# Performance work log

Measured on AMD Instinct MI355X. Metric: run time of the kernel, lower is better.

The kernel has to match this reference:

```python
import jax, jax.numpy as jnp
import numpy as np
from jax import lax

B, T, F = 64, 100, 128
HD = [32, 64]            # encoder hidden dims; decoder uses reversed [64, 32]
KH, KW = 3, 3


def _conv(x, w):
    # x: (b, cin, f, 1), w: (cout, cin, kh, kw), SAME padding
    ph, pw = w.shape[2] // 2, w.shape[3] // 2
    return lax.conv_general_dilated(x, w, (1, 1), [(ph, ph), (pw, pw)],
                                    dimension_numbers=("NCHW", "OIHW", "NCHW"))


def _run_layer(xs, h0, wg, bg, wc, bc):
    # xs: (t, b, cin, f, 1); h0: (b, hd, f, 1)
    def step(h, x):
        g = _conv(jnp.concatenate([x, h], axis=1), wg) + bg[None, :, None, None]
        r, u = jnp.split(jax.nn.sigmoid(g), 2, axis=1)
        c = jnp.tanh(_conv(jnp.concatenate([x, r * h], axis=1), wc) + bc[None, :, None, None])
        h_next = (1.0 - u) * h + u * c
        return h_next, h_next
    h_last, ys = lax.scan(step, h0, xs)
    return ys, h_last


def setup_inputs() -> dict:
    key = jax.random.key(0)
    ks = iter(jax.random.split(key, 32))
    s = 0.05
    d = {"x": jax.random.normal(next(ks), (B, T, F), dtype=jnp.float32)}
    # encoder: layer0 in=1 hd=32, layer1 in=32 hd=64
    # decoder: input_dim=64, hidden reversed [64,32]: layer0 in=64 hd=64, layer1 in=64 hd=32
    specs = {
        "e0": (1, 32), "e1": (32, 64),
        "d0": (64, 64), "d1": (64, 32),
    }
    for name, (cin, hd) in specs.items():
        d[name + "_wg"] = jax.random.normal(next(ks), (2 * hd, cin + hd, KH, KW), dtype=jnp.float32) * s
        d[name + "_bg"] = jnp.zeros((2 * hd,), dtype=jnp.float32)
        d[name + "_wc"] = jax.random.normal(next(ks), (hd, cin + hd, KH, KW), dtype=jnp.float32) * s
        d[name + "_bc"] = jnp.zeros((hd,), dtype=jnp.float32)
    d["fw"] = jax.random.normal(next(ks), (1, 32, 1, 1), dtype=jnp.float32) * s
    d["fb"] = jnp.zeros((1,), dtype=jnp.float32)
    return d


def reference(x,
              e0_wg, e0_bg, e0_wc, e0_bc,
              e1_wg, e1_bg, e1_wc, e1_bc,
              d0_wg, d0_bg, d0_wc, d0_bc,
              d1_wg, d1_bg, d1_wc, d1_bc,
              fw, fb):
    b, t, f = x.shape
    xs = x.reshape(b, t, 1, f, 1).transpose(1, 0, 2, 3, 4)  # (t,b,1,f,1)
    zeros = lambda hd: jnp.zeros((b, hd, f, 1), dtype=x.dtype)
    # encoder (return_all_layers; decoder consumes last layer output)
    y0, h0 = _run_layer(xs, zeros(HD[0]), e0_wg, e0_bg, e0_wc, e0_bc)
    y1, h1 = _run_layer(y0, zeros(HD[1]), e1_wg, e1_bg, e1_wc, e1_bc)
    # decoder init states = encoder last states reversed: [h1 (64ch), h0 (32ch)]
    z0, _ = _run_layer(y1, h1, d0_wg, d0_bg, d0_wc, d0_bc)
    z1, _ = _run_layer(z0, h0, d1_wg, d1_bg, d1_wc, d1_bc)
    # final 1x1 conv: (t,b,32,f,1) x (1,32) -> (t,b,1,f,1)
    rec = jnp.einsum("tbcfw,oc->tbofw", z1, fw[:, :, 0, 0]) + fb[None, None, :, None, None]
    return rec.transpose(1, 0, 2, 3, 4).reshape(b, t, f)
```

## Files before the change

kernel.cpp:

```cpp
#include <hip/hip_runtime.h>
#include <cstdint>
#include <cstddef>


#define F_ 128
#define T_ 100
#define B_ 64
#define ROWSP 130
#define CBSTR (ROWSP * 8)
#define CBBYTE (ROWSP * 16)
#define AT_OFF 104448
#define LDS_TOTAL (AT_OFF + 28 * CBBYTE)

typedef _Float16 f16;
typedef __attribute__((ext_vector_type(4))) float f32x4;
typedef __attribute__((ext_vector_type(8))) _Float16 f16x8;
typedef __attribute__((ext_vector_type(4))) _Float16 f16x4;

#define MFMA(a, b, c) __builtin_amdgcn_mfma_f32_16x16x32_f16(a, b, c, 0, 0, 0)

__device__ __forceinline__ float exp2_(float x) { return __builtin_amdgcn_exp2f(x); }
__device__ __forceinline__ float rcp_(float x) { return __builtin_amdgcn_rcpf(x); }

#define KSG (-1.442695041f)
#define KTH (-2.885390082f)

__host__ __device__ constexpr int cbA(int lid, int km) {
  return lid == 0 ? (km ? 4 : 0)
       : lid == 1 ? (1 + km * 4)
       : lid == 2 ? (km * 4)
                  : (8 + km * 4);
}
__host__ __device__ constexpr int cbB(int lid, int km) {
  return lid == 0 ? (km ? 17 : 13)
       : lid == 1 ? (km == 0 ? 1 : 14 + km * 4)
       : lid == 2 ? (km < 2 ? km * 4 : 12 + km * 4)
                  : (km < 2 ? 8 + km * 4 : 20);
}

template <int LID, int FTW, int NK, int NC3, bool WREG>
__device__ __forceinline__ void convA_f(
    const f16* __restrict__ rdB,
    const f16x8* __restrict__ aR, const f16x8* __restrict__ aU,
    const f16* __restrict__ gR, const f16* __restrict__ gU,
    f32x4* __restrict__ accR, f32x4* __restrict__ accU) {
#pragma unroll
  for (int j = 0; j < FTW; ++j) {
    accR[j] = (f32x4){0.f, 0.f, 0.f, 0.f};
    accU[j] = (f32x4){0.f, 0.f, 0.f, 0.f};
  }
#pragma unroll
  for (int ks = 0; ks < NK; ++ks) {
    const int k = ks / NC3, km = ks % NC3;
    const f16* fb = rdB + cbA(LID, km) * CBSTR + k * 8;
    f16x8 bf[FTW];
#pragma unroll
    for (int j = 0; j < FTW; ++j) bf[j] = *(const f16x8*)(fb + j * 128);
    f16x8 wr, wu;
    if constexpr (WREG) { wr = aR[ks]; wu = aU[ks]; }
    else {
      wr = *(const f16x8*)(gR + ks * 512);
      wu = *(const f16x8*)(gU + ks * 512);
    }
#pragma unroll
    for (int j = 0; j < FTW; ++j) accR[j] = MFMA(wr, bf[j], accR[j]);
#pragma unroll
    for (int j = 0; j < FTW; ++j) accU[j] = MFMA(wu, bf[j], accU[j]);
  }
}

template <int LID, int FTW, int NK, int NC3, bool CREG>
__device__ __forceinline__ void convB_f(
    const f16* __restrict__ rdB, const f16x8* __restrict__ cR,
    const f16* __restrict__ cW, f32x4* __restrict__ accC) {
#pragma unroll
  for (int j = 0; j < FTW; ++j) accC[j] = (f32x4){0.f, 0.f, 0.f, 0.f};
#pragma unroll
  for (int ks = 0; ks < NK; ++ks) {
    const int k = ks / NC3, km = ks % NC3;
    const f16* fb = rdB + cbB(LID, km) * CBSTR + k * 8;
    f16x8 bf[FTW];
#pragma unroll
    for (int j = 0; j < FTW; ++j) bf[j] = *(const f16x8*)(fb + j * 128);
    f16x8 wc;
    if constexpr (CREG) wc = cR[ks];
    else wc = *(const f16x8*)(cW + ks * 512);
#pragma unroll
    for (int j = 0; j < FTW; ++j) accC[j] = MFMA(wc, bf[j], accC[j]);
  }
}

template <int FTW, int RHCB>
__device__ __forceinline__ void postA_f(const f32x4* __restrict__ accR,
                                        const f32x4 bR,
                                        const f32x4* __restrict__ hreg,
                                        char* __restrict__ wrB) {
#pragma unroll
  for (int j = 0; j < FTW; ++j) {
    f16x4 rh;
#pragma unroll
    for (int q = 0; q < 4; ++q) {
      const float r = rcp_(1.0f + exp2_(fmaf(accR[j][q], KSG, bR[q])));
      rh[q] = (f16)(r * hreg[j][q]);
    }
    *(f16x4*)(wrB + RHCB * CBBYTE + j * 256) = rh;
  }
}

template <int FTW, int HCB, bool EMITY1>
__device__ __forceinline__ void postB_f(const f32x4* __restrict__ accU,
                                        const f32x4* __restrict__ accC,
                                        const f32x4 bU, const f32x4 bC,
                                        f32x4* __restrict__ hreg,
                                        char* __restrict__ wrB,
                                        f16* __restrict__ y1dst) {
#pragma unroll
  for (int j = 0; j < FTW; ++j) {
    f16x4 hh;
#pragma unroll
    for (int q = 0; q < 4; ++q) {
      const float u = rcp_(1.0f + exp2_(fmaf(accU[j][q], KSG, bU[q])));
      const float r = rcp_(1.0f + exp2_(fmaf(accC[j][q], KTH, bC[q])));
      const float h = hreg[j][q];
      const float s = fmaf(2.0f, r, -(1.0f + h));
      const float hn = fmaf(u, s, h);
      hreg[j][q] = hn;
      hh[q] = (f16)hn;
    }
    *(f16x4*)(wrB + HCB * CBBYTE + j * 256) = hh;
    if constexpr (EMITY1) *(f16x4*)(y1dst + j * 128) = hh;
  }
}

__global__ __launch_bounds__(512, 1) void ae_kernel(
    const f16* __restrict__ xf, float* __restrict__ out,
    const f16* __restrict__ wgE0, const f16* __restrict__ wcE0,
    const float* __restrict__ bgE0, const float* __restrict__ bcE0,
    const f16* __restrict__ wgE1, const f16* __restrict__ wcE1,
    const float* __restrict__ bgE1, const float* __restrict__ bcE1,
    const f16* __restrict__ wgD0, const f16* __restrict__ wcD0,
    const float* __restrict__ bgD0, const float* __restrict__ bcD0,
    const f16* __restrict__ wgD1, const f16* __restrict__ wcD1,
    const float* __restrict__ bgD1, const float* __restrict__ bcD1,
    const float* __restrict__ fw, const float* __restrict__ fb,
    f16* __restrict__ y1g) {
  extern __shared__ char smem[];
  f16* aT = (f16*)(smem + AT_OFF);
  const int tid = threadIdx.x, b = blockIdx.x;
  const int w = tid >> 6, l = tid & 63;
  const int m16 = l & 15, kb = l >> 4;

  for (int i = tid; i < 28 * CBBYTE / 16; i += 512)
    ((f32x4*)(smem + AT_OFF))[i] = (f32x4){0.f, 0.f, 0.f, 0.f};
  for (int i = tid; i < 1536; i += 512)
    ((f16x8*)(smem + 0))[i] = ((const f16x8*)wgE0)[i];
  for (int i = tid; i < 768; i += 512)
    ((f16x8*)(smem + 24576))[i] = ((const f16x8*)wcE0)[i];

  const int cot2 = w & 1, cot4 = w & 3;
  f16x8 aR1[9], aU1[9], cE1[9];
#pragma unroll
  for (int ks = 0; ks < 9; ++ks) {
    aR1[ks] = ((const f16x8*)wgE1)[(cot4 * 9 + ks) * 64 + l];
    aU1[ks] = ((const f16x8*)wgE1)[((cot4 + 4) * 9 + ks) * 64 + l];
    cE1[ks] = ((const f16x8*)wcE1)[(cot4 * 9 + ks) * 64 + l];
  }
  const int co2 = cot2 * 16 + kb * 4;
  const int co4 = cot4 * 16 + kb * 4;
  f32x4 bRe0, bUe0, bCe0, bRe1, bUe1, bCe1;
#pragma unroll
  for (int q = 0; q < 4; ++q) {
    bRe0[q] = bgE0[co2 + q] * KSG;
    bUe0[q] = bgE0[32 + co2 + q] * KSG;
    bCe0[q] = bcE0[co2 + q] * KTH;
    bRe1[q] = bgE1[co4 + q] * KSG;
    bUe1[q] = bgE1[64 + co4 + q] * KSG;
    bCe1[q] = bcE1[co4 + q] * KTH;
  }
  const int ft2 = (w >> 1) * 2, ft4 = (w >> 2) * 4;
  const f16* rdB2 = aT + kb * CBSTR + (ft2 * 16 + m16) * 8;
  const f16* rdB4 = aT + kb * CBSTR + (ft4 * 16 + m16) * 8;
  char* wrB2 = (char*)aT + (cot2 * 2 + (kb >> 1)) * CBBYTE +
               (ft2 * 16 + m16 + 1) * 16 + (kb & 1) * 8;
  char* wrB4 = (char*)aT + (cot4 * 2 + (kb >> 1)) * CBBYTE +
               (ft4 * 16 + m16 + 1) * 16 + (kb & 1) * 8;
  f16* y1t = y1g + (size_t)b * T_ * 8192 +
             ((cot4 * 2 + (kb >> 1)) * 128 + ft4 * 16 + m16) * 8 + (kb & 1) * 4;
  const f16* gE0R = (const f16*)(smem + 0) + (cot2 * 6) * 512 + l * 8;
  const f16* gE0U = (const f16*)(smem + 0) + ((2 + cot2) * 6) * 512 + l * 8;
  const f16* cE0l = (const f16*)(smem + 24576) + (cot2 * 6) * 512 + l * 8;

  f32x4 h0r[2], h1r[4];
#pragma unroll
  for (int j = 0; j < 2; ++j) h0r[j] = (f32x4){0.f, 0.f, 0.f, 0.f};
#pragma unroll
  for (int j = 0; j < 4; ++j) h1r[j] = (f32x4){0.f, 0.f, 0.f, 0.f};
  __syncthreads();

  const f16* xb = xf + (size_t)b * T_ * F_;
  if (tid < F_) {
    const f16 v = xb[tid];
    aT[(tid + 1) * 8] = v;
    aT[13 * CBSTR + (tid + 1) * 8] = v;
  }
  __syncthreads();
  for (int t = 0; t < T_; ++t) {
    f32x4 aR0g[2], aU0g[2];
    convA_f<0, 2, 6, 2, false>(rdB2, nullptr, nullptr, gE0R, gE0U, aR0g, aU0g);
    f16 xpre = (f16)0.f;
    if (t + 1 < T_ && tid < F_) xpre = xb[(t + 1) * F_ + tid];
    postA_f<2, 14>(aR0g, bRe0, h0r, wrB2);
    __syncthreads();
    f32x4 aC0[2];
    convB_f<0, 2, 6, 2, false>(rdB2, nullptr, cE0l, aC0);
    postB_f<2, 1, false>(aU0g, aC0, bUe0, bCe0, h0r, wrB2, nullptr);
    __syncthreads();
    f32x4 aR1g[4], aU1g[4];
    convA_f<1, 4, 9, 3, true>(rdB4, aR1, aU1, nullptr, nullptr, aR1g, aU1g);
    if (t + 1 < T_ && tid < F_) {
      aT[(tid + 1) * 8] = xpre;
      aT[13 * CBSTR + (tid + 1) * 8] = xpre;
    }
    postA_f<4, 18>(aR1g, bRe1, h1r, wrB4);
    __syncthreads();
    f32x4 aC1[4];
    convB_f<1, 4, 9, 3, true>(rdB4, cE1, nullptr, aC1);
    postB_f<4, 5, true>(aU1g, aC1, bUe1, bCe1, h1r, wrB4,
                        y1t + (size_t)t * 8192);
    __syncthreads();
  }

  {
#pragma unroll
    for (int j = 0; j < 4; ++j) {
      f16x4 hh;
#pragma unroll
      for (int q = 0; q < 4; ++q) hh[q] = (f16)h1r[j][q];
      *(f16x4*)(wrB4 + 8 * CBBYTE + j * 256) = hh;
    }
#pragma unroll
    for (int j = 0; j < 2; ++j) {
      f16x4 hh;
#pragma unroll
      for (int q = 0; q < 4; ++q) hh[q] = (f16)h0r[j][q];
      *(f16x4*)(wrB2 + 16 * CBBYTE + j * 256) = hh;
    }
  }
  for (int i = tid; i < 3072; i += 512)
    ((f16x8*)(smem + 0))[i] = ((const f16x8*)wcD0)[i];
  for (int i = tid; i < 2304; i += 512)
    ((f16x8*)(smem + 49152))[i] = ((const f16x8*)wgD1)[i];
  for (int i = tid; i < 1152; i += 512)
    ((f16x8*)(smem + 86016))[i] = ((const f16x8*)wcD1)[i];
  f16x8 aR0[12], aU0[12];
#pragma unroll
  for (int ks = 0; ks < 12; ++ks) {
    aR0[ks] = ((const f16x8*)wgD0)[(cot4 * 12 + ks) * 64 + l];
    aU0[ks] = ((const f16x8*)wgD0)[((cot4 + 4) * 12 + ks) * 64 + l];
  }
  f32x4 bRd0, bUd0, bCd0, bRd1, bUd1, bCd1;
#pragma unroll
  for (int q = 0; q < 4; ++q) {
    bRd0[q] = bgD0[co4 + q] * KSG;
    bUd0[q] = bgD0[64 + co4 + q] * KSG;
    bCd0[q] = bcD0[co4 + q] * KTH;
    bRd1[q] = bgD1[co2 + q] * KSG;
    bUd1[q] = bgD1[32 + co2 + q] * KSG;
    bCd1[q] = bcD1[co2 + q] * KTH;
  }
  const f16* cD0l = (const f16*)(smem + 0) + (cot4 * 12) * 512 + l * 8;
  const f16* gD1R = (const f16*)(smem + 49152) + (cot2 * 9) * 512 + l * 8;
  const f16* gD1U = (const f16*)(smem + 49152) + ((2 + cot2) * 9) * 512 + l * 8;
  const f16* cD1l = (const f16*)(smem + 86016) + (cot2 * 9) * 512 + l * 8;
  const float fb0 = fb[0];
  __syncthreads();
  {
    const f16x8* src = (const f16x8*)(y1g + (size_t)b * T_ * 8192);
#pragma unroll
    for (int k2 = 0; k2 < 2; ++k2) {
      const int i = tid + k2 * 512;
      *(f16x8*)&aT[(i >> 7) * CBSTR + ((i & 127) + 1) * 8] = src[i];
    }
  }
  __syncthreads();

  for (int t = 0; t < T_; ++t) {
    f32x4 aRd0[4], aUd0[4];
    convA_f<2, 4, 12, 4, true>(rdB4, aR0, aU0, nullptr, nullptr, aRd0, aUd0);
    if (t >= 1 && tid < F_) {
      float s = fb0;
#pragma unroll
      for (int cb = 0; cb < 4; ++cb) {
        const f16x8 h8 = *(const f16x8*)&aT[(16 + cb) * CBSTR + (tid + 1) * 8];
#pragma unroll
        for (int q = 0; q < 8; ++q) s = fmaf(fw[cb * 8 + q], (float)h8[q], s);
      }
      out[((size_t)b * T_ + (t - 1)) * F_ + tid] = s;
    }
    f16x8 yp0 = {}, yp1 = {};
    if (t + 1 < T_) {
      const f16x8* src = (const f16x8*)(y1g + ((size_t)b * T_ + t + 1) * 8192);
      yp0 = src[tid];
      yp1 = src[tid + 512];
    }
    postA_f<4, 20>(aRd0, bRd0, h1r, wrB4);
    __syncthreads();
    f32x4 aCd0[4];
    convB_f<2, 4, 12, 4, false>(rdB4, nullptr, cD0l, aCd0);
    postB_f<4, 8, false>(aUd0, aCd0, bUd0, bCd0, h1r, wrB4, nullptr);
    __syncthreads();
    f32x4 aRd1[2], aUd1[2];
    convA_f<3, 2, 9, 3, false>(rdB2, nullptr, nullptr, gD1R, gD1U, aRd1, aUd1);
    if (t + 1 < T_) {
      const int i0 = tid, i1 = tid + 512;
      *(f16x8*)&aT[(i0 >> 7) * CBSTR + ((i0 & 127) + 1) * 8] = yp0;
      *(f16x8*)&aT[(i1 >> 7) * CBSTR + ((i1 & 127) + 1) * 8] = yp1;
    }
    postA_f<2, 20>(aRd1, bRd1, h0r, wrB2);
    __syncthreads();
    f32x4 aCd1[2];
    convB_f<3, 2, 9, 3, false>(rdB2, nullptr, cD1l, aCd1);
    postB_f<2, 16, false>(aUd1, aCd1, bUd1, bCd1, h0r, wrB2, nullptr);
    __syncthreads();
  }
  if (tid < F_) {
    float s = fb0;
#pragma unroll
    for (int cb = 0; cb < 4; ++cb) {
      const f16x8 h8 = *(const f16x8*)&aT[(16 + cb) * CBSTR + (tid + 1) * 8];
#pragma unroll
      for (int q = 0; q < 8; ++q) s = fmaf(fw[cb * 8 + q], (float)h8[q], s);
    }
    out[((size_t)b * T_ + (T_ - 1)) * F_ + tid] = s;
  }
}

__global__ void repack_f16(const float* __restrict__ src, f16* __restrict__ dst,
                           int CO, int CI, int CINH, int NK, int e0map) {
  const int n = (CO / 16) * NK * 64;
  for (int i = blockIdx.x * blockDim.x + threadIdx.x; i < n;
       i += gridDim.x * blockDim.x) {
    const int cot = i / (NK * 64);
    const int r = i - cot * NK * 64;
    const int ks = r >> 6, lph = r & 63;
    const int co = cot * 16 + (lph & 15);
    const int kbl = lph >> 4;
#pragma unroll
    for (int j = 0; j < 8; ++j) {
      const int kk = ks * 32 + kbl * 8 + j;
      const int k = kk / CINH, c = kk - k * CINH;
      int ci;
      if (e0map) ci = (c == 0) ? 0 : ((c >= 8 && c < 40) ? c - 7 : -1);
      else ci = (c < CI) ? c : -1;
      float wv = 0.f;
      if (ci >= 0) wv = src[((size_t)(co * CI + ci) * 3 + k) * 3 + 1];
      dst[(size_t)i * 8 + j] = (f16)wv;
    }
  }
}

__global__ void xcvt(const float* __restrict__ x, f16* __restrict__ xf, int n4) {
  for (int i = blockIdx.x * blockDim.x + threadIdx.x; i < n4;
       i += gridDim.x * blockDim.x) {
    const float4 v = ((const float4*)x)[i];
    f16x4 o;
    o[0] = (f16)v.x; o[1] = (f16)v.y; o[2] = (f16)v.z; o[3] = (f16)v.w;
    ((f16x4*)xf)[i] = o;
  }
}

extern "C" void kernel_launch(void* const* d_in, const int* in_sizes, int n_in,
                              void* d_out, int out_size, void* d_ws, size_t ws_size,
                              hipStream_t stream) {
  (void)in_sizes; (void)n_in; (void)out_size; (void)ws_size;
  const float* x = (const float*)d_in[0];
  const float* e0_wg = (const float*)d_in[1];
  const float* e0_bg = (const float*)d_in[2];
  const float* e0_wc = (const float*)d_in[3];
  const float* e0_bc = (const float*)d_in[4];
  const float* e1_wg = (const float*)d_in[5];
  const float* e1_bg = (const float*)d_in[6];
  const float* e1_wc = (const float*)d_in[7];
  const float* e1_bc = (const float*)d_in[8];
  const float* d0_wg = (const float*)d_in[9];
  const float* d0_bg = (const float*)d_in[10];
  const float* d0_wc = (const float*)d_in[11];
  const float* d0_bc = (const float*)d_in[12];
  const float* d1_wg = (const float*)d_in[13];
  const float* d1_bg = (const float*)d_in[14];
  const float* d1_wc = (const float*)d_in[15];
  const float* d1_bc = (const float*)d_in[16];
  const float* fw = (const float*)d_in[17];
  const float* fb = (const float*)d_in[18];
  float* out = (float*)d_out;

  char* p = (char*)d_ws;
  f16* y1g = (f16*)p;
  p += (size_t)B_ * T_ * 64 * 128 * 2;
  f16* xf = (f16*)p;
  p += (size_t)B_ * T_ * F_ * 2;
  auto aw = [&](int n) { f16* q = (f16*)p; p += (size_t)n * 2; return q; };
  f16* wgE0 = aw(64 * 192);
  f16* wcE0 = aw(32 * 192);
  f16* wgE1 = aw(128 * 288);
  f16* wcE1 = aw(64 * 288);
  f16* wgD0 = aw(128 * 384);
  f16* wcD0 = aw(64 * 384);
  f16* wgD1 = aw(64 * 288);
  f16* wcD1 = aw(32 * 288);

  auto rp = [&](const float* s, f16* d, int CO, int CI, int CINH, int e0m) {
    const int NK = 3 * CINH / 32;
    const int n = (CO / 16) * NK * 64;
    hipLaunchKernelGGL(repack_f16, dim3((n + 255) / 256), dim3(256), 0, stream,
                       s, d, CO, CI, CINH, NK, e0m);
  };
  rp(e0_wg, wgE0, 64, 33, 64, 1);
  rp(e0_wc, wcE0, 32, 33, 64, 1);
  rp(e1_wg, wgE1, 128, 96, 96, 0);
  rp(e1_wc, wcE1, 64, 96, 96, 0);
  rp(d0_wg, wgD0, 128, 128, 128, 0);
  rp(d0_wc, wcD0, 64, 128, 128, 0);
  rp(d1_wg, wgD1, 64, 96, 96, 0);
  rp(d1_wc, wcD1, 32, 96, 96, 0);
  hipLaunchKernelGGL(xcvt, dim3(200), dim3(1024), 0, stream, x, xf,
                     B_ * T_ * F_ / 4);

  hipFuncSetAttribute((const void*)ae_kernel,
                      hipFuncAttributeMaxDynamicSharedMemorySize, LDS_TOTAL);
  hipLaunchKernelGGL(ae_kernel, dim3(B_), dim3(512), LDS_TOTAL, stream, xf, out,
                     wgE0, wcE0, e0_bg, e0_bc, wgE1, wcE1, e1_bg, e1_bc,
                     wgD0, wcD0, d0_bg, d0_bc, wgD1, wcD1, d1_bg, d1_bc,
                     fw, fb, y1g);
}
```

Measured before the change: 1.166 ms.

## Skew layer pipelines to merge candidate phase of one layer with next step's gate phase

Within each of the encoder and decoder loops, the candidate conv and update of the second layer are deferred into the next timestep so they run in the same barrier phase as the first layer's gate conv. This cuts barriers per timestep from four to three. The r*h buffers are relocated to extra LDS channel blocks so both phases can coexist. The decoder layer-1 candidate weights move from LDS into registers, which raises register pressure. The skew needs a prologue/epilogue step and careful buffer separation to stay correct.

Result: slower. 1.280 ms (+9.7%).

```diff
diff --git a/kernel.cpp b/kernel.cpp
--- a/kernel.cpp
+++ b/kernel.cpp
@@ -9,8 +9,9 @@
 #define ROWSP 130
 #define CBSTR (ROWSP * 8)
 #define CBBYTE (ROWSP * 16)
-#define AT_OFF 104448
-#define LDS_TOTAL (AT_OFF + 28 * CBBYTE)
+#define AT_OFF 86016
+#define NCB 32
+#define LDS_TOTAL (AT_OFF + NCB * CBBYTE)
 
 typedef _Float16 f16;
 typedef __attribute__((ext_vector_type(4))) float f32x4;
@@ -27,15 +28,15 @@
 
 __host__ __device__ constexpr int cbA(int lid, int km) {
   return lid == 0 ? (km ? 4 : 0)
-       : lid == 1 ? (1 + km * 4)
-       : lid == 2 ? (km * 4)
-                  : (8 + km * 4);
+       : lid == 1 ? (km == 0 ? 1 : 4 + 4 * km)
+       : lid == 2 ? (4 * km)
+                  : (8 + 4 * km);
 }
 __host__ __device__ constexpr int cbB(int lid, int km) {
-  return lid == 0 ? (km ? 17 : 13)
-       : lid == 1 ? (km == 0 ? 1 : 14 + km * 4)
-       : lid == 2 ? (km < 2 ? km * 4 : 12 + km * 4)
-                  : (km < 2 ? 8 + km * 4 : 20);
+  return lid == 0 ? (km ? 20 : 16)
+       : lid == 1 ? (km == 0 ? 1 : 20 + 4 * km)
+       : lid == 2 ? (km < 2 ? 4 * km : 12 + 4 * km)
+                  : (km < 2 ? 8 + 4 * km : 28);
 }
 
 template <int LID, int FTW, int NK, int NC3, bool WREG>
@@ -150,7 +151,7 @@
   const int w = tid >> 6, l = tid & 63;
   const int m16 = l & 15, kb = l >> 4;
 
-  for (int i = tid; i < 28 * CBBYTE / 16; i += 512)
+  for (int i = tid; i < NCB * CBBYTE / 16; i += 512)
     ((f32x4*)(smem + AT_OFF))[i] = (f32x4){0.f, 0.f, 0.f, 0.f};
   for (int i = tid; i < 1536; i += 512)
     ((f16x8*)(smem + 0))[i] = ((const f16x8*)wgE0)[i];
@@ -201,43 +202,38 @@
   if (tid < F_) {
     const f16 v = xb[tid];
     aT[(tid + 1) * 8] = v;
-    aT[13 * CBSTR + (tid + 1) * 8] = v;
-  }
-  __syncthreads();
+    aT[16 * CBSTR + (tid + 1) * 8] = v;
+  }
+  __syncthreads();
+  f32x4 aU1g[4], aR1g[4];
   for (int t = 0; t < T_; ++t) {
-    f32x4 aR0g[2], aU0g[2];
+    f32x4 aC1[4], aR0g[2], aU0g[2];
+    if (t > 0) convB_f<1, 4, 9, 3, true>(rdB4, cE1, nullptr, aC1);
     convA_f<0, 2, 6, 2, false>(rdB2, nullptr, nullptr, gE0R, gE0U, aR0g, aU0g);
+    if (t > 0)
+      postB_f<4, 8, true>(aU1g, aC1, bUe1, bCe1, h1r, wrB4,
+                          y1t + (size_t)(t - 1) * 8192);
+    postA_f<2, 17>(aR0g, bRe0, h0r, wrB2);
+    __syncthreads();
+    f32x4 aC0[2];
+    convB_f<0, 2, 6, 2, false>(rdB2, nullptr, cE0l, aC0);
     f16 xpre = (f16)0.f;
     if (t + 1 < T_ && tid < F_) xpre = xb[(t + 1) * F_ + tid];
-    postA_f<2, 14>(aR0g, bRe0, h0r, wrB2);
-    __syncthreads();
-    f32x4 aC0[2];
-    convB_f<0, 2, 6, 2, false>(rdB2, nullptr, cE0l, aC0);
     postB_f<2, 1, false>(aU0g, aC0, bUe0, bCe0, h0r, wrB2, nullptr);
     __syncthreads();
-    f32x4 aR1g[4], aU1g[4];
     convA_f<1, 4, 9, 3, true>(rdB4, aR1, aU1, nullptr, nullptr, aR1g, aU1g);
     if (t + 1 < T_ && tid < F_) {
       aT[(tid + 1) * 8] = xpre;
-      aT[13 * CBSTR + (tid + 1) * 8] = xpre;
-    }
-    postA_f<4, 18>(aR1g, bRe1, h1r, wrB4);
-    __syncthreads();
+      aT[16 * CBSTR + (tid + 1) * 8] = xpre;
+    }
+    postA_f<4, 24>(aR1g, bRe1, h1r, wrB4);
+    __syncthreads();
+  }
+  {
     f32x4 aC1[4];
     convB_f<1, 4, 9, 3, true>(rdB4, cE1, nullptr, aC1);
-    postB_f<4, 5, true>(aU1g, aC1, bUe1, bCe1, h1r, wrB4,
-                        y1t + (size_t)t * 8192);
-    __syncthreads();
-  }
-
-  {
-#pragma unroll
-    for (int j = 0; j < 4; ++j) {
-      f16x4 hh;
-#pragma unroll
-      for (int q = 0; q < 4; ++q) hh[q] = (f16)h1r[j][q];
-      *(f16x4*)(wrB4 + 8 * CBBYTE + j * 256) = hh;
-    }
+    postB_f<4, 8, true>(aU1g, aC1, bUe1, bCe1, h1r, wrB4,
+                        y1t + (size_t)(T_ - 1) * 8192);
 #pragma unroll
     for (int j = 0; j < 2; ++j) {
       f16x4 hh;
@@ -246,18 +242,21 @@
       *(f16x4*)(wrB2 + 16 * CBBYTE + j * 256) = hh;
     }
   }
+  __syncthreads();
+
   for (int i = tid; i < 3072; i += 512)
     ((f16x8*)(smem + 0))[i] = ((const f16x8*)wcD0)[i];
   for (int i = tid; i < 2304; i += 512)
     ((f16x8*)(smem + 49152))[i] = ((const f16x8*)wgD1)[i];
-  for (int i = tid; i < 1152; i += 512)
-    ((f16x8*)(smem + 86016))[i] = ((const f16x8*)wcD1)[i];
-  f16x8 aR0[12], aU0[12];
+  f16x8 aR0[12], aU0[12], wCd1[9];
 #pragma unroll
   for (int ks = 0; ks < 12; ++ks) {
     aR0[ks] = ((const f16x8*)wgD0)[(cot4 * 12 + ks) * 64 + l];
     aU0[ks] = ((const f16x8*)wgD0)[((cot4 + 4) * 12 + ks) * 64 + l];
   }
+#pragma unroll
+  for (int ks = 0; ks < 9; ++ks)
+    wCd1[ks] = ((const f16x8*)wcD1)[(cot2 * 9 + ks) * 64 + l];
   f32x4 bRd0, bUd0, bCd0, bRd1, bUd1, bCd1;
 #pragma unroll
   for (int q = 0; q < 4; ++q) {
@@ -268,10 +267,9 @@
     bUd1[q] = bgD1[32 + co2 + q] * KSG;
     bCd1[q] = bcD1[co2 + q] * KTH;
   }
-  const f16* cD0l = (const f16*)(smem + 0) + (cot4 * 12) * 512 + l * 8;
   const f16* gD1R = (const f16*)(smem + 49152) + (cot2 * 9) * 512 + l * 8;
   const f16* gD1U = (const f16*)(smem + 49152) + ((2 + cot2) * 9) * 512 + l * 8;
-  const f16* cD1l = (const f16*)(smem + 86016) + (cot2 * 9) * 512 + l * 8;
+  const f16* cD0l = (const f16*)(smem + 0) + (cot4 * 12) * 512 + l * 8;
   const float fb0 = fb[0];
   __syncthreads();
   {
@@ -284,45 +282,49 @@
   }
   __syncthreads();
 
+  f32x4 aUd1[2], aRd1[2];
   for (int t = 0; t < T_; ++t) {
-    f32x4 aRd0[4], aUd0[4];
+    f32x4 aCd1[2], aRd0[4], aUd0[4];
+    if (t > 0) convB_f<3, 2, 9, 3, true>(rdB2, wCd1, nullptr, aCd1);
     convA_f<2, 4, 12, 4, true>(rdB4, aR0, aU0, nullptr, nullptr, aRd0, aUd0);
-    if (t >= 1 && tid < F_) {
-      float s = fb0;
-#pragma unroll
-      for (int cb = 0; cb < 4; ++cb) {
-        const f16x8 h8 = *(const f16x8*)&aT[(16 + cb) * CBSTR + (tid + 1) * 8];
-#pragma unroll
-        for (int q = 0; q < 8; ++q) s = fmaf(fw[cb * 8 + q], (float)h8[q], s);
-      }
-      out[((size_t)b * T_ + (t - 1)) * F_ + tid] = s;
-    }
     f16x8 yp0 = {}, yp1 = {};
     if (t + 1 < T_) {
       const f16x8* src = (const f16x8*)(y1g + ((size_t)b * T_ + t + 1) * 8192);
       yp0 = src[tid];
       yp1 = src[tid + 512];
     }
+    if (t > 0) postB_f<2, 16, false>(aUd1, aCd1, bUd1, bCd1, h0r, wrB2, nullptr);
     postA_f<4, 20>(aRd0, bRd0, h1r, wrB4);
     __syncthreads();
     f32x4 aCd0[4];
     convB_f<2, 4, 12, 4, false>(rdB4, nullptr, cD0l, aCd0);
+    if (t >= 1 && tid < F_) {
+      float s = fb0;
+#pragma unroll
+      for (int cb = 0; cb < 4; ++cb) {
+        const f16x8 h8 = *(const f16x8*)&aT[(16 + cb) * CBSTR + (tid + 1) * 8];
+#pragma unroll
+        for (int q = 0; q < 8; ++q) s = fmaf(fw[cb * 8 + q], (float)h8[q], s);
+      }
+      out[((size_t)b * T_ + (t - 1)) * F_ + tid] = s;
+    }
     postB_f<4, 8, false>(aUd0, aCd0, bUd0, bCd0, h1r, wrB4, nullptr);
     __syncthreads();
-    f32x4 aRd1[2], aUd1[2];
     convA_f<3, 2, 9, 3, false>(rdB2, nullptr, nullptr, gD1R, gD1U, aRd1, aUd1);
     if (t + 1 < T_) {
       const int i0 = tid, i1 = tid + 512;
       *(f16x8*)&aT[(i0 >> 7) * CBSTR + ((i0 & 127) + 1) * 8] = yp0;
       *(f16x8*)&aT[(i1 >> 7) * CBSTR + ((i1 & 127) + 1) * 8] = yp1;
     }
-    postA_f<2, 20>(aRd1, bRd1, h0r, wrB2);
-    __syncthreads();
+    postA_f<2, 28>(aRd1, bRd1, h0r, wrB2);
+    __syncthreads();
+  }
+  {
     f32x4 aCd1[2];
-    convB_f<3, 2, 9, 3, false>(rdB2, nullptr, cD1l, aCd1);
+    convB_f<3, 2, 9, 3, true>(rdB2, wCd1, nullptr, aCd1);
     postB_f<2, 16, false>(aUd1, aCd1, bUd1, bCd1, h0r, wrB2, nullptr);
-    __syncthreads();
-  }
+  }
+  __syncthreads();
   if (tid < F_) {
     float s = fb0;
 #pragma unroll
```

## Double block to 1024 threads and halve frequency tiles per wave

Applied to the files above, without the earlier changes.

The block size goes from 512 to 1024 threads, and each wave now handles half as many frequency tiles in every GRU layer step. The per-layer register arrays, tile offsets and staging loops are rescaled to match. This is meant to shorten the serial per-timestep critical path, since only 64 blocks run and each block's recurrence is latency-bound. In exchange, more waves share each CU's register file while the large register-resident weight fragments stay the same size, so register spilling or lower ILP is a risk, and barriers now synchronize twice as many waves.

After: 2.092 ms. +79.4%, slower.

```diff
diff --git a/kernel.cpp b/kernel.cpp
--- a/kernel.cpp
+++ b/kernel.cpp
@@ -132,7 +132,7 @@
   }
 }
 
-__global__ __launch_bounds__(512, 1) void ae_kernel(
+__global__ __launch_bounds__(1024, 1) void ae_kernel(
     const f16* __restrict__ xf, float* __restrict__ out,
     const f16* __restrict__ wgE0, const f16* __restrict__ wcE0,
     const float* __restrict__ bgE0, const float* __restrict__ bcE0,
@@ -150,14 +150,16 @@
   const int w = tid >> 6, l = tid & 63;
   const int m16 = l & 15, kb = l >> 4;
 
-  for (int i = tid; i < 28 * CBBYTE / 16; i += 512)
+  for (int i = tid; i < 28 * CBBYTE / 16; i += 1024)
     ((f32x4*)(smem + AT_OFF))[i] = (f32x4){0.f, 0.f, 0.f, 0.f};
-  for (int i = tid; i < 1536; i += 512)
+  for (int i = tid; i < 1536; i += 1024)
     ((f16x8*)(smem + 0))[i] = ((const f16x8*)wgE0)[i];
-  for (int i = tid; i < 768; i += 512)
+  for (int i = tid; i < 768; i += 1024)
     ((f16x8*)(smem + 24576))[i] = ((const f16x8*)wcE0)[i];
 
   const int cot2 = w & 1, cot4 = w & 3;
+  const int ft1 = w >> 1;
+  const int ftg2 = w >> 2;
   f16x8 aR1[9], aU1[9], cE1[9];
 #pragma unroll
   for (int ks = 0; ks < 9; ++ks) {
@@ -177,24 +179,22 @@
     bUe1[q] = bgE1[64 + co4 + q] * KSG;
     bCe1[q] = bcE1[co4 + q] * KTH;
   }
-  const int ft2 = (w >> 1) * 2, ft4 = (w >> 2) * 4;
-  const f16* rdB2 = aT + kb * CBSTR + (ft2 * 16 + m16) * 8;
-  const f16* rdB4 = aT + kb * CBSTR + (ft4 * 16 + m16) * 8;
+  const f16* rdB2 = aT + kb * CBSTR + (ft1 * 16 + m16) * 8;
+  const f16* rdB4 = aT + kb * CBSTR + (ftg2 * 32 + m16) * 8;
   char* wrB2 = (char*)aT + (cot2 * 2 + (kb >> 1)) * CBBYTE +
-               (ft2 * 16 + m16 + 1) * 16 + (kb & 1) * 8;
+               (ft1 * 16 + m16 + 1) * 16 + (kb & 1) * 8;
   char* wrB4 = (char*)aT + (cot4 * 2 + (kb >> 1)) * CBBYTE +
-               (ft4 * 16 + m16 + 1) * 16 + (kb & 1) * 8;
+               (ftg2 * 32 + m16 + 1) * 16 + (kb & 1) * 8;
   f16* y1t = y1g + (size_t)b * T_ * 8192 +
-             ((cot4 * 2 + (kb >> 1)) * 128 + ft4 * 16 + m16) * 8 + (kb & 1) * 4;
+             ((cot4 * 2 + (kb >> 1)) * 128 + ftg2 * 32 + m16) * 8 + (kb & 1) * 4;
   const f16* gE0R = (const f16*)(smem + 0) + (cot2 * 6) * 512 + l * 8;
   const f16* gE0U = (const f16*)(smem + 0) + ((2 + cot2) * 6) * 512 + l * 8;
   const f16* cE0l = (const f16*)(smem + 24576) + (cot2 * 6) * 512 + l * 8;
 
-  f32x4 h0r[2], h1r[4];
-#pragma unroll
-  for (int j = 0; j < 2; ++j) h0r[j] = (f32x4){0.f, 0.f, 0.f, 0.f};
-#pragma unroll
-  for (int j = 0; j < 4; ++j) h1r[j] = (f32x4){0.f, 0.f, 0.f, 0.f};
+  f32x4 h0r[1], h1r[2];
+  h0r[0] = (f32x4){0.f, 0.f, 0.f, 0.f};
+#pragma unroll
+  for (int j = 0; j < 2; ++j) h1r[j] = (f32x4){0.f, 0.f, 0.f, 0.f};
   __syncthreads();
 
   const f16* xb = xf + (size_t)b * T_ * F_;
@@ -205,52 +205,51 @@
   }
   __syncthreads();
   for (int t = 0; t < T_; ++t) {
-    f32x4 aR0g[2], aU0g[2];
-    convA_f<0, 2, 6, 2, false>(rdB2, nullptr, nullptr, gE0R, gE0U, aR0g, aU0g);
+    f32x4 aR0g[1], aU0g[1];
+    convA_f<0, 1, 6, 2, false>(rdB2, nullptr, nullptr, gE0R, gE0U, aR0g, aU0g);
     f16 xpre = (f16)0.f;
     if (t + 1 < T_ && tid < F_) xpre = xb[(t + 1) * F_ + tid];
-    postA_f<2, 14>(aR0g, bRe0, h0r, wrB2);
-    __syncthreads();
-    f32x4 aC0[2];
-    convB_f<0, 2, 6, 2, false>(rdB2, nullptr, cE0l, aC0);
-    postB_f<2, 1, false>(aU0g, aC0, bUe0, bCe0, h0r, wrB2, nullptr);
-    __syncthreads();
-    f32x4 aR1g[4], aU1g[4];
-    convA_f<1, 4, 9, 3, true>(rdB4, aR1, aU1, nullptr, nullptr, aR1g, aU1g);
+    postA_f<1, 14>(aR0g, bRe0, h0r, wrB2);
+    __syncthreads();
+    f32x4 aC0[1];
+    convB_f<0, 1, 6, 2, false>(rdB2, nullptr, cE0l, aC0);
+    postB_f<1, 1, false>(aU0g, aC0, bUe0, bCe0, h0r, wrB2, nullptr);
+    __syncthreads();
+    f32x4 aR1g[2], aU1g[2];
+    convA_f<1, 2, 9, 3, true>(rdB4, aR1, aU1, nullptr, nullptr, aR1g, aU1g);
     if (t + 1 < T_ && tid < F_) {
       aT[(tid + 1) * 8] = xpre;
       aT[13 * CBSTR + (tid + 1) * 8] = xpre;
     }
-    postA_f<4, 18>(aR1g, bRe1, h1r, wrB4);
-    __syncthreads();
-    f32x4 aC1[4];
-    convB_f<1, 4, 9, 3, true>(rdB4, cE1, nullptr, aC1);
-    postB_f<4, 5, true>(aU1g, aC1, bUe1, bCe1, h1r, wrB4,
+    postA_f<2, 18>(aR1g, bRe1, h1r, wrB4);
+    __syncthreads();
+    f32x4 aC1[2];
+    convB_f<1, 2, 9, 3, true>(rdB4, cE1, nullptr, aC1);
+    postB_f<2, 5, true>(aU1g, aC1, bUe1, bCe1, h1r, wrB4,
                         y1t + (size_t)t * 8192);
     __syncthreads();
   }
 
   {
 #pragma unroll
-    for (int j = 0; j < 4; ++j) {
+    for (int j = 0; j < 2; ++j) {
       f16x4 hh;
 #pragma unroll
       for (int q = 0; q < 4; ++q) hh[q] = (f16)h1r[j][q];
       *(f16x4*)(wrB4 + 8 * CBBYTE + j * 256) = hh;
     }
-#pragma unroll
-    for (int j = 0; j < 2; ++j) {
+    {
       f16x4 hh;
 #pragma unroll
-      for (int q = 0; q < 4; ++q) hh[q] = (f16)h0r[j][q];
-      *(f16x4*)(wrB2 + 16 * CBBYTE + j * 256) = hh;
-    }
-  }
-  for (int i = tid; i < 3072; i += 512)
+      for (int q = 0; q < 4; ++q) hh[q] = (f16)h0r[0][q];
+      *(f16x4*)(wrB2 + 16 * CBBYTE) = hh;
+    }
+  }
+  for (int i = tid; i < 3072; i += 1024)
     ((f16x8*)(smem + 0))[i] = ((const f16x8*)wcD0)[i];
-  for (int i = tid; i < 2304; i += 512)
+  for (int i = tid; i < 2304; i += 1024)
     ((f16x8*)(smem + 49152))[i] = ((const f16x8*)wgD1)[i];
-  for (int i = tid; i < 1152; i += 512)
+  for (int i = tid; i < 1152; i += 1024)
     ((f16x8*)(smem + 86016))[i] = ((const f16x8*)wcD1)[i];
   f16x8 aR0[12], aU0[12];
 #pragma unroll
@@ -276,17 +275,13 @@
   __syncthreads();
   {
     const f16x8* src = (const f16x8*)(y1g + (size_t)b * T_ * 8192);
-#pragma unroll
-    for (int k2 = 0; k2 < 2; ++k2) {
-      const int i = tid + k2 * 512;
-      *(f16x8*)&aT[(i >> 7) * CBSTR + ((i & 127) + 1) * 8] = src[i];
-    }
+    *(f16x8*)&aT[(tid >> 7) * CBSTR + ((tid & 127) + 1) * 8] = src[tid];
   }
   __syncthreads();
 
   for (int t = 0; t < T_; ++t) {
-    f32x4 aRd0[4], aUd0[4];
-    convA_f<2, 4, 12, 4, true>(rdB4, aR0, aU0, nullptr, nullptr, aRd0, aUd0);
+    f32x4 aRd0[2], aUd0[2];
+    convA_f<2, 2, 12, 4, true>(rdB4, aR0, aU0, nullptr, nullptr, aRd0, aUd0);
     if (t >= 1 && tid < F_) {
       float s = fb0;
 #pragma unroll
@@ -297,30 +292,26 @@
       }
       out[((size_t)b * T_ + (t - 1)) * F_ + tid] = s;
     }
-    f16x8 yp0 = {}, yp1 = {};
+    f16x8 yp0 = {};
     if (t + 1 < T_) {
       const f16x8* src = (const f16x8*)(y1g + ((size_t)b * T_ + t + 1) * 8192);
       yp0 = src[tid];
-      yp1 = src[tid + 512];
-    }
-    postA_f<4, 20>(aRd0, bRd0, h1r, wrB4);
-    __syncthreads();
-    f32x4 aCd0[4];
-    convB_f<2, 4, 12, 4, false>(rdB4, nullptr, cD0l, aCd0);
-    postB_f<4, 8, false>(aUd0, aCd0, bUd0, bCd0, h1r, wrB4, nullptr);
-    __syncthreads();
-    f32x4 aRd1[2], aUd1[2];
-    convA_f<3, 2, 9, 3, false>(rdB2, nullptr, nullptr, gD1R, gD1U, aRd1, aUd1);
-    if (t + 1 < T_) {
-      const int i0 = tid, i1 = tid + 512;
-      *(f16x8*)&aT[(i0 >> 7) * CBSTR + ((i0 & 127) + 1) * 8] = yp0;
-      *(f16x8*)&aT[(i1 >> 7) * CBSTR + ((i1 & 127) + 1) * 8] = yp1;
-    }
-    postA_f<2, 20>(aRd1, bRd1, h0r, wrB2);
-    __syncthreads();
-    f32x4 aCd1[2];
-    convB_f<3, 2, 9, 3, false>(rdB2, nullptr, cD1l, aCd1);
-    postB_f<2, 16, false>(aUd1, aCd1, bUd1, bCd1, h0r, wrB2, nullptr);
+    }
+    postA_f<2, 20>(aRd0, bRd0, h1r, wrB4);
+    __syncthreads();
+    f32x4 aCd0[2];
+    convB_f<2, 2, 12, 4, false>(rdB4, nullptr, cD0l, aCd0);
+    postB_f<2, 8, false>(aUd0, aCd0, bUd0, bCd0, h1r, wrB4, nullptr);
+    __syncthreads();
+    f32x4 aRd1[1], aUd1[1];
+    convA_f<3, 1, 9, 3, false>(rdB2, nullptr, nullptr, gD1R, gD1U, aRd1, aUd1);
+    if (t + 1 < T_)
+      *(f16x8*)&aT[(tid >> 7) * CBSTR + ((tid & 127) + 1) * 8] = yp0;
+    postA_f<1, 20>(aRd1, bRd1, h0r, wrB2);
+    __syncthreads();
+    f32x4 aCd1[1];
+    convB_f<3, 1, 9, 3, false>(rdB2, nullptr, cD1l, aCd1);
+    postB_f<1, 16, false>(aUd1, aCd1, bUd1, bCd1, h0r, wrB2, nullptr);
     __syncthreads();
   }
   if (tid < F_) {
@@ -428,7 +419,7 @@
 
   hipFuncSetAttribute((const void*)ae_kernel,
                       hipFuncAttributeMaxDynamicSharedMemorySize, LDS_TOTAL);
-  hipLaunchKernelGGL(ae_kernel, dim3(B_), dim3(512), LDS_TOTAL, stream, xf, out,
+  hipLaunchKernelGGL(ae_kernel, dim3(B_), dim3(1024), LDS_TOTAL, stream, xf, out,
                      wgE0, wcE0, e0_bg, e0_bc, wgE1, wcE1, e1_bg, e1_bc,
                      wgD0, wcD0, d0_bg, d0_bc, wgD1, wcD1, d1_bg, d1_bc,
                      fw, fb, y1g);
```

## Retile 64-channel layers to 2 channel tiles x 2 feature tiles per wave

Applied to the files above, without the earlier changes.

For the 64-hidden-channel layers (encoder layer 1, decoder layer 0), each wave now covers two output-channel tiles and two 16-row feature tiles instead of one channel tile and four feature tiles. Each B fragment read from LDS is reused across two weight tiles, and all layers share a single read pointer. The aim is to halve the LDS B-operand loads per MFMA in the heavier layers. The cost is doubled per-wave register-resident weights (18 to 24 f16x8 arrays each), which raises register pressure and could cause spills under the 512-thread launch bound.

Measured after the change: 1.843 ms. +58.0%, slower.

```diff
diff --git a/kernel.cpp b/kernel.cpp
--- a/kernel.cpp
+++ b/kernel.cpp
@@ -130,6 +130,108 @@
     *(f16x4*)(wrB + HCB * CBBYTE + j * 256) = hh;
     if constexpr (EMITY1) *(f16x4*)(y1dst + j * 128) = hh;
   }
+}
+
+template <int LID, int NK, int NC3>
+__device__ __forceinline__ void convA2_f(const f16* __restrict__ rdB,
+                                         const f16x8* __restrict__ aR,
+                                         const f16x8* __restrict__ aU,
+                                         f32x4* __restrict__ accR,
+                                         f32x4* __restrict__ accU) {
+#pragma unroll
+  for (int t = 0; t < 4; ++t) {
+    accR[t] = (f32x4){0.f, 0.f, 0.f, 0.f};
+    accU[t] = (f32x4){0.f, 0.f, 0.f, 0.f};
+  }
+#pragma unroll
+  for (int ks = 0; ks < NK; ++ks) {
+    const int k = ks / NC3, km = ks % NC3;
+    const f16* fb = rdB + cbA(LID, km) * CBSTR + k * 8;
+    const f16x8 b0 = *(const f16x8*)(fb);
+    const f16x8 b1 = *(const f16x8*)(fb + 128);
+#pragma unroll
+    for (int i = 0; i < 2; ++i) {
+      const f16x8 wr = aR[i * NK + ks];
+      const f16x8 wu = aU[i * NK + ks];
+      accR[i * 2 + 0] = MFMA(wr, b0, accR[i * 2 + 0]);
+      accR[i * 2 + 1] = MFMA(wr, b1, accR[i * 2 + 1]);
+      accU[i * 2 + 0] = MFMA(wu, b0, accU[i * 2 + 0]);
+      accU[i * 2 + 1] = MFMA(wu, b1, accU[i * 2 + 1]);
+    }
+  }
+}
+
+template <int LID, int NK, int NC3, bool CREG>
+__device__ __forceinline__ void convB2_f(const f16* __restrict__ rdB,
+                                         const f16x8* __restrict__ cR,
+                                         const f16* __restrict__ cW,
+                                         f32x4* __restrict__ accC) {
+#pragma unroll
+  for (int t = 0; t < 4; ++t) accC[t] = (f32x4){0.f, 0.f, 0.f, 0.f};
+#pragma unroll
+  for (int ks = 0; ks < NK; ++ks) {
+    const int k = ks / NC3, km = ks % NC3;
+    const f16* fb = rdB + cbB(LID, km) * CBSTR + k * 8;
+    const f16x8 b0 = *(const f16x8*)(fb);
+    const f16x8 b1 = *(const f16x8*)(fb + 128);
+#pragma unroll
+    for (int i = 0; i < 2; ++i) {
+      f16x8 wc;
+      if constexpr (CREG) wc = cR[i * NK + ks];
+      else wc = *(const f16x8*)(cW + (i * NK + ks) * 512);
+      accC[i * 2 + 0] = MFMA(wc, b0, accC[i * 2 + 0]);
+      accC[i * 2 + 1] = MFMA(wc, b1, accC[i * 2 + 1]);
+    }
+  }
+}
+
+template <int RHCB>
+__device__ __forceinline__ void postA2_f(const f32x4* __restrict__ accR,
+                                         const f32x4* __restrict__ bR2,
+                                         const f32x4* __restrict__ hreg,
+                                         char* __restrict__ wrB) {
+#pragma unroll
+  for (int i = 0; i < 2; ++i)
+#pragma unroll
+    for (int j = 0; j < 2; ++j) {
+      const int t = i * 2 + j;
+      f16x4 rh;
+#pragma unroll
+      for (int q = 0; q < 4; ++q) {
+        const float r = rcp_(1.0f + exp2_(fmaf(accR[t][q], KSG, bR2[i][q])));
+        rh[q] = (f16)(r * hreg[t][q]);
+      }
+      *(f16x4*)(wrB + RHCB * CBBYTE + i * 2 * CBBYTE + j * 256) = rh;
+    }
+}
+
+template <int HCB, bool EMITY1>
+__device__ __forceinline__ void postB2_f(const f32x4* __restrict__ accU,
+                                         const f32x4* __restrict__ accC,
+                                         const f32x4* __restrict__ bU2,
+                                         const f32x4* __restrict__ bC2,
+                                         f32x4* __restrict__ hreg,
+                                         char* __restrict__ wrB,
+                                         f16* __restrict__ y1dst) {
+#pragma unroll
+  for (int i = 0; i < 2; ++i)
+#pragma unroll
+    for (int j = 0; j < 2; ++j) {
+      const int t = i * 2 + j;
+      f16x4 hh;
+#pragma unroll
+      for (int q = 0; q < 4; ++q) {
+        const float u = rcp_(1.0f + exp2_(fmaf(accU[t][q], KSG, bU2[i][q])));
+        const float r = rcp_(1.0f + exp2_(fmaf(accC[t][q], KTH, bC2[i][q])));
+        const float h = hreg[t][q];
+        const float s = fmaf(2.0f, r, -(1.0f + h));
+        const float hn = fmaf(u, s, h);
+        hreg[t][q] = hn;
+        hh[q] = (f16)hn;
+      }
+      *(f16x4*)(wrB + HCB * CBBYTE + i * 2 * CBBYTE + j * 256) = hh;
+      if constexpr (EMITY1) *(f16x4*)(y1dst + i * 2048 + j * 128) = hh;
+    }
 }
 
 __global__ __launch_bounds__(512, 1) void ae_kernel(
@@ -146,49 +248,54 @@
     f16* __restrict__ y1g) {
   extern __shared__ char smem[];
   f16* aT = (f16*)(smem + AT_OFF);
+  char* atB = smem + AT_OFF;
   const int tid = threadIdx.x, b = blockIdx.x;
   const int w = tid >> 6, l = tid & 63;
   const int m16 = l & 15, kb = l >> 4;
+  const int cp = w & 1, fg2 = w >> 1;
 
   for (int i = tid; i < 28 * CBBYTE / 16; i += 512)
-    ((f32x4*)(smem + AT_OFF))[i] = (f32x4){0.f, 0.f, 0.f, 0.f};
+    ((f32x4*)atB)[i] = (f32x4){0.f, 0.f, 0.f, 0.f};
   for (int i = tid; i < 1536; i += 512)
     ((f16x8*)(smem + 0))[i] = ((const f16x8*)wgE0)[i];
   for (int i = tid; i < 768; i += 512)
     ((f16x8*)(smem + 24576))[i] = ((const f16x8*)wcE0)[i];
 
-  const int cot2 = w & 1, cot4 = w & 3;
-  f16x8 aR1[9], aU1[9], cE1[9];
-#pragma unroll
-  for (int ks = 0; ks < 9; ++ks) {
-    aR1[ks] = ((const f16x8*)wgE1)[(cot4 * 9 + ks) * 64 + l];
-    aU1[ks] = ((const f16x8*)wgE1)[((cot4 + 4) * 9 + ks) * 64 + l];
-    cE1[ks] = ((const f16x8*)wcE1)[(cot4 * 9 + ks) * 64 + l];
-  }
-  const int co2 = cot2 * 16 + kb * 4;
-  const int co4 = cot4 * 16 + kb * 4;
-  f32x4 bRe0, bUe0, bCe0, bRe1, bUe1, bCe1;
+  f16x8 aR1[18], aU1[18], cE1[18];
+#pragma unroll
+  for (int i = 0; i < 2; ++i)
+#pragma unroll
+    for (int ks = 0; ks < 9; ++ks) {
+      aR1[i * 9 + ks] = ((const f16x8*)wgE1)[((2 * cp + i) * 9 + ks) * 64 + l];
+      aU1[i * 9 + ks] =
+          ((const f16x8*)wgE1)[((2 * cp + i + 4) * 9 + ks) * 64 + l];
+      cE1[i * 9 + ks] = ((const f16x8*)wcE1)[((2 * cp + i) * 9 + ks) * 64 + l];
+    }
+  const int kb4 = kb * 4;
+  const int co2 = cp * 16 + kb4;
+  const int coA = (2 * cp) * 16 + kb4, coB = (2 * cp + 1) * 16 + kb4;
+  f32x4 bRe0, bUe0, bCe0, bRe1[2], bUe1[2], bCe1[2];
 #pragma unroll
   for (int q = 0; q < 4; ++q) {
     bRe0[q] = bgE0[co2 + q] * KSG;
     bUe0[q] = bgE0[32 + co2 + q] * KSG;
     bCe0[q] = bcE0[co2 + q] * KTH;
-    bRe1[q] = bgE1[co4 + q] * KSG;
-    bUe1[q] = bgE1[64 + co4 + q] * KSG;
-    bCe1[q] = bcE1[co4 + q] * KTH;
-  }
-  const int ft2 = (w >> 1) * 2, ft4 = (w >> 2) * 4;
-  const f16* rdB2 = aT + kb * CBSTR + (ft2 * 16 + m16) * 8;
-  const f16* rdB4 = aT + kb * CBSTR + (ft4 * 16 + m16) * 8;
-  char* wrB2 = (char*)aT + (cot2 * 2 + (kb >> 1)) * CBBYTE +
-               (ft2 * 16 + m16 + 1) * 16 + (kb & 1) * 8;
-  char* wrB4 = (char*)aT + (cot4 * 2 + (kb >> 1)) * CBBYTE +
-               (ft4 * 16 + m16 + 1) * 16 + (kb & 1) * 8;
+    bRe1[0][q] = bgE1[coA + q] * KSG;
+    bRe1[1][q] = bgE1[coB + q] * KSG;
+    bUe1[0][q] = bgE1[64 + coA + q] * KSG;
+    bUe1[1][q] = bgE1[64 + coB + q] * KSG;
+    bCe1[0][q] = bcE1[coA + q] * KTH;
+    bCe1[1][q] = bcE1[coB + q] * KTH;
+  }
+  const int rowb = (fg2 * 32 + m16 + 1) * 16 + (kb & 1) * 8;
+  const f16* rdB = aT + kb * CBSTR + (fg2 * 32 + m16) * 8;
+  char* wrB2 = atB + (cp * 2 + (kb >> 1)) * CBBYTE + rowb;
+  char* wrB4 = atB + (4 * cp + (kb >> 1)) * CBBYTE + rowb;
   f16* y1t = y1g + (size_t)b * T_ * 8192 +
-             ((cot4 * 2 + (kb >> 1)) * 128 + ft4 * 16 + m16) * 8 + (kb & 1) * 4;
-  const f16* gE0R = (const f16*)(smem + 0) + (cot2 * 6) * 512 + l * 8;
-  const f16* gE0U = (const f16*)(smem + 0) + ((2 + cot2) * 6) * 512 + l * 8;
-  const f16* cE0l = (const f16*)(smem + 24576) + (cot2 * 6) * 512 + l * 8;
+             ((4 * cp + (kb >> 1)) * 128 + fg2 * 32 + m16) * 8 + (kb & 1) * 4;
+  const f16* gE0R = (const f16*)(smem + 0) + (cp * 6) * 512 + l * 8;
+  const f16* gE0U = (const f16*)(smem + 0) + ((2 + cp) * 6) * 512 + l * 8;
+  const f16* cE0l = (const f16*)(smem + 24576) + (cp * 6) * 512 + l * 8;
 
   f32x4 h0r[2], h1r[4];
 #pragma unroll
@@ -206,38 +313,40 @@
   __syncthreads();
   for (int t = 0; t < T_; ++t) {
     f32x4 aR0g[2], aU0g[2];
-    convA_f<0, 2, 6, 2, false>(rdB2, nullptr, nullptr, gE0R, gE0U, aR0g, aU0g);
+    convA_f<0, 2, 6, 2, false>(rdB, nullptr, nullptr, gE0R, gE0U, aR0g, aU0g);
     f16 xpre = (f16)0.f;
     if (t + 1 < T_ && tid < F_) xpre = xb[(t + 1) * F_ + tid];
     postA_f<2, 14>(aR0g, bRe0, h0r, wrB2);
     __syncthreads();
     f32x4 aC0[2];
-    convB_f<0, 2, 6, 2, false>(rdB2, nullptr, cE0l, aC0);
+    convB_f<0, 2, 6, 2, false>(rdB, nullptr, cE0l, aC0);
     postB_f<2, 1, false>(aU0g, aC0, bUe0, bCe0, h0r, wrB2, nullptr);
     __syncthreads();
     f32x4 aR1g[4], aU1g[4];
-    convA_f<1, 4, 9, 3, true>(rdB4, aR1, aU1, nullptr, nullptr, aR1g, aU1g);
+    convA2_f<1, 9, 3>(rdB, aR1, aU1, aR1g, aU1g);
     if (t + 1 < T_ && tid < F_) {
       aT[(tid + 1) * 8] = xpre;
       aT[13 * CBSTR + (tid + 1) * 8] = xpre;
     }
-    postA_f<4, 18>(aR1g, bRe1, h1r, wrB4);
+    postA2_f<18>(aR1g, bRe1, h1r, wrB4);
     __syncthreads();
     f32x4 aC1[4];
-    convB_f<1, 4, 9, 3, true>(rdB4, cE1, nullptr, aC1);
-    postB_f<4, 5, true>(aU1g, aC1, bUe1, bCe1, h1r, wrB4,
-                        y1t + (size_t)t * 8192);
+    convB2_f<1, 9, 3, true>(rdB, cE1, nullptr, aC1);
+    postB2_f<5, true>(aU1g, aC1, bUe1, bCe1, h1r, wrB4,
+                      y1t + (size_t)t * 8192);
     __syncthreads();
   }
 
   {
 #pragma unroll
-    for (int j = 0; j < 4; ++j) {
-      f16x4 hh;
-#pragma unroll
-      for (int q = 0; q < 4; ++q) hh[q] = (f16)h1r[j][q];
-      *(f16x4*)(wrB4 + 8 * CBBYTE + j * 256) = hh;
-    }
+    for (int i = 0; i < 2; ++i)
+#pragma unroll
+      for (int j = 0; j < 2; ++j) {
+        f16x4 hh;
+#pragma unroll
+        for (int q = 0; q < 4; ++q) hh[q] = (f16)h1r[i * 2 + j][q];
+        *(f16x4*)(wrB4 + 8 * CBBYTE + i * 2 * CBBYTE + j * 256) = hh;
+      }
 #pragma unroll
     for (int j = 0; j < 2; ++j) {
       f16x4 hh;
@@ -252,26 +361,33 @@
     ((f16x8*)(smem + 49152))[i] = ((const f16x8*)wgD1)[i];
   for (int i = tid; i < 1152; i += 512)
     ((f16x8*)(smem + 86016))[i] = ((const f16x8*)wcD1)[i];
-  f16x8 aR0[12], aU0[12];
-#pragma unroll
-  for (int ks = 0; ks < 12; ++ks) {
-    aR0[ks] = ((const f16x8*)wgD0)[(cot4 * 12 + ks) * 64 + l];
-    aU0[ks] = ((const f16x8*)wgD0)[((cot4 + 4) * 12 + ks) * 64 + l];
-  }
-  f32x4 bRd0, bUd0, bCd0, bRd1, bUd1, bCd1;
+  f16x8 aR0[24], aU0[24];
+#pragma unroll
+  for (int i = 0; i < 2; ++i)
+#pragma unroll
+    for (int ks = 0; ks < 12; ++ks) {
+      aR0[i * 12 + ks] =
+          ((const f16x8*)wgD0)[((2 * cp + i) * 12 + ks) * 64 + l];
+      aU0[i * 12 + ks] =
+          ((const f16x8*)wgD0)[((2 * cp + i + 4) * 12 + ks) * 64 + l];
+    }
+  f32x4 bRd0[2], bUd0[2], bCd0[2], bRd1, bUd1, bCd1;
 #pragma unroll
   for (int q = 0; q < 4; ++q) {
-    bRd0[q] = bgD0[co4 + q] * KSG;
-    bUd0[q] = bgD0[64 + co4 + q] * KSG;
-    bCd0[q] = bcD0[co4 + q] * KTH;
+    bRd0[0][q] = bgD0[coA + q] * KSG;
+    bRd0[1][q] = bgD0[coB + q] * KSG;
+    bUd0[0][q] = bgD0[64 + coA + q] * KSG;
+    bUd0[1][q] = bgD0[64 + coB + q] * KSG;
+    bCd0[0][q] = bcD0[coA + q] * KTH;
+    bCd0[1][q] = bcD0[coB + q] * KTH;
     bRd1[q] = bgD1[co2 + q] * KSG;
     bUd1[q] = bgD1[32 + co2 + q] * KSG;
     bCd1[q] = bcD1[co2 + q] * KTH;
   }
-  const f16* cD0l = (const f16*)(smem + 0) + (cot4 * 12) * 512 + l * 8;
-  const f16* gD1R = (const f16*)(smem + 49152) + (cot2 * 9) * 512 + l * 8;
-  const f16* gD1U = (const f16*)(smem + 49152) + ((2 + cot2) * 9) * 512 + l * 8;
-  const f16* cD1l = (const f16*)(smem + 86016) + (cot2 * 9) * 512 + l * 8;
+  const f16* cD0l = (const f16*)(smem + 0) + (2 * cp * 12) * 512 + l * 8;
+  const f16* gD1R = (const f16*)(smem + 49152) + (cp * 9) * 512 + l * 8;
+  const f16* gD1U = (const f16*)(smem + 49152) + ((2 + cp) * 9) * 512 + l * 8;
+  const f16* cD1l = (const f16*)(smem + 86016) + (cp * 9) * 512 + l * 8;
   const float fb0 = fb[0];
   __syncthreads();
   {
@@ -286,7 +402,7 @@
 
   for (int t = 0; t < T_; ++t) {
     f32x4 aRd0[4], aUd0[4];
-    convA_f<2, 4, 12, 4, true>(rdB4, aR0, aU0, nullptr, nullptr, aRd0, aUd0);
+    convA2_f<2, 12, 4>(rdB, aR0, aU0, aRd0, aUd0);
     if (t >= 1 && tid < F_) {
       float s = fb0;
 #pragma unroll
@@ -303,14 +419,14 @@
       yp0 = src[tid];
       yp1 = src[tid + 512];
     }
-    postA_f<4, 20>(aRd0, bRd0, h1r, wrB4);
+    postA2_f<20>(aRd0, bRd0, h1r, wrB4);
     __syncthreads();
     f32x4 aCd0[4];
-    convB_f<2, 4, 12, 4, false>(rdB4, nullptr, cD0l, aCd0);
-    postB_f<4, 8, false>(aUd0, aCd0, bUd0, bCd0, h1r, wrB4, nullptr);
+    convB2_f<2, 12, 4, false>(rdB, nullptr, cD0l, aCd0);
+    postB2_f<8, false>(aUd0, aCd0, bUd0, bCd0, h1r, wrB4, nullptr);
     __syncthreads();
     f32x4 aRd1[2], aUd1[2];
-    convA_f<3, 2, 9, 3, false>(rdB2, nullptr, nullptr, gD1R, gD1U, aRd1, aUd1);
+    convA_f<3, 2, 9, 3, false>(rdB, nullptr, nullptr, gD1R, gD1U, aRd1, aUd1);
     if (t + 1 < T_) {
       const int i0 = tid, i1 = tid + 512;
       *(f16x8*)&aT[(i0 >> 7) * CBSTR + ((i0 & 127) + 1) * 8] = yp0;
@@ -319,7 +435,7 @@
     postA_f<2, 20>(aRd1, bRd1, h0r, wrB2);
     __syncthreads();
     f32x4 aCd1[2];
-    convB_f<3, 2, 9, 3, false>(rdB2, nullptr, cD1l, aCd1);
+    convB_f<3, 2, 9, 3, false>(rdB, nullptr, cD1l, aCd1);
     postB_f<2, 16, false>(aUd1, aCd1, bUd1, bCd1, h0r, wrB2, nullptr);
     __syncthreads();
   }
```
